# Kernel tuning notes

Hardware: AMD Instinct MI355X
Metric: run time of the kernel (lower is better)

The kernel has to match this reference:

```python
import jax, jax.numpy as jnp
import numpy as np

N = 8192      # num nodes
D = 128       # feature dim (input_dim)
E = 262144    # num edges (avg degree 32)
P = 4         # num perspectives (num_pers)
EPSILON = 0.3 # similarity threshold (args.epsilon)


def setup_inputs() -> dict:
    key = jax.random.key(0)
    k1, k2, k3, k4 = jax.random.split(key, 4)
    x = jax.random.normal(k1, (N, D), dtype=jnp.float32)
    ori_index = jax.random.randint(k2, (2, E), 0, N, dtype=jnp.int32)
    ori_weight = jax.random.uniform(k3, (E,), dtype=jnp.float32)
    w_pers = jax.random.normal(k4, (P, D), dtype=jnp.float32)  # weighted-cosine perspective weights
    return {"x": x, "ori_index": ori_index, "ori_weight": ori_weight, "w_pers": w_pers}


def reference(x, ori_index, ori_weight, w_pers):
    n = x.shape[0]
    # to_dense_adj: scatter edge weights into dense [N, N] adjacency (duplicate edges add)
    ori_g = jnp.zeros((n, n), dtype=x.dtype).at[ori_index[0], ori_index[1]].add(ori_weight)

    # GraphLearner (weighted multi-perspective cosine):
    # reweight features per perspective, L2-normalize, cosine sim, mean over perspectives
    xw = x[None, :, :] * w_pers[:, None, :]                              # [P, N, D]
    xn = xw / jnp.maximum(jnp.linalg.norm(xw, axis=-1, keepdims=True), 1e-12)
    sim = jnp.mean(jnp.einsum('pnd,pmd->pnm', xn, xn), axis=0)           # [N, N]
    # epsilon-thresholded learned graph
    sim_g = jnp.where(sim > EPSILON, sim, jnp.zeros_like(sim))

    # purified(sim, ori_g, epsilon): keep original edges where sim*ori_g > epsilon
    pur_g = jnp.where(sim * ori_g > EPSILON, ori_g, jnp.zeros_like(sim))
    new_g = pur_g + sim_g
    # dense_to_sparse has data-dependent output size; return the dense refined
    # adjacency (same information: edges = nonzero(new_g), weights = values).
    return new_g
```

## Files before the change

kernel.cpp:

```cpp
#include <hip/hip_runtime.h>
#include <hip/hip_bf16.h>
#include <stdint.h>

#define N_NODES 8192
#define DIM     128
#define KTOT    512
#define NEDGE   262144
#define EPS     0.3f
#define FIX_DELTA 0.0043f
#define FIX_CAP (1u << 19)
#define XCAP    (1u << 18)
#define LCAP    512
#define HASH_BITS 19
#define HASH_SLOTS (1u << HASH_BITS)

typedef unsigned int u32;
typedef unsigned short u16;
typedef __attribute__((ext_vector_type(8))) short short8;
typedef __attribute__((ext_vector_type(4))) float float4v;

#define OFF_YF  0u
#define OFF_YB  16777216u
#define OFF_CTR 25165824u
#define OFF_HK  25166080u
#define OFF_HV  27263232u
#define OFF_FL  29360384u
#define OFF_UL  31457536u
#define OFF_XL  32506112u
#define ZERO_VEC4 262160u

__device__ __forceinline__ u16 f2bf(float f) {
    u32 b = __builtin_bit_cast(u32, f);
    b += 0x7fffu + ((b >> 16) & 1u);
    return (u16)(b >> 16);
}

__global__ void prep_y(const float* __restrict__ x, const float* __restrict__ wp,
                       float* __restrict__ yf, u16* __restrict__ yb,
                       uint4* __restrict__ zbase) {
    if (blockIdx.x >= 2048) {
        for (u32 idx = (blockIdx.x - 2048) * 256 + threadIdx.x; idx < ZERO_VEC4;
             idx += 512 * 256)
            zbase[idx] = make_uint4(0, 0, 0, 0);
        return;
    }
    int node = blockIdx.x * 4 + (threadIdx.x >> 6);
    int lane = threadIdx.x & 63;
    float x0 = x[node * DIM + lane];
    float x1 = x[node * DIM + lane + 64];
    for (int p = 0; p < 4; ++p) {
        float v0 = x0 * wp[p * DIM + lane];
        float v1 = x1 * wp[p * DIM + lane + 64];
        float ss = v0 * v0 + v1 * v1;
        #pragma unroll
        for (int o = 1; o < 64; o <<= 1) ss += __shfl_xor(ss, o, 64);
        float scale = 0.5f / fmaxf(sqrtf(ss), 1e-12f);
        float y0 = v0 * scale, y1 = v1 * scale;
        int base = node * KTOT + p * DIM;
        yf[base + lane] = y0;       yf[base + lane + 64] = y1;
        yb[base + lane] = f2bf(y0); yb[base + lane + 64] = f2bf(y1);
    }
}

__global__ void edge_insert(const int* __restrict__ idx, const float* __restrict__ w,
                            u32* __restrict__ hkey, float* __restrict__ hval,
                            u32* __restrict__ ucnt, u32* __restrict__ ulist) {
    int e = blockIdx.x * 256 + threadIdx.x;
    u32 cell = (u32)(idx[e] * N_NODES + idx[NEDGE + e]);
    float wv = w[e];
    u32 key = cell + 1u;
    u32 h = (cell * 2654435761u) >> (32 - HASH_BITS);
    while (true) {
        u32 old = atomicCAS(&hkey[h], 0u, key);
        if (old == 0u) { ulist[atomicAdd(ucnt, 1u)] = h; atomicAdd(&hval[h], wv); break; }
        if (old == key) { atomicAdd(&hval[h], wv); break; }
        h = (h + 1u) & (HASH_SLOTS - 1u);
    }
}

#define TM  128
#define BK  64
#define TLD 132

__global__ __launch_bounds__(512)
void gemm_sim(const u16* __restrict__ yb, float* __restrict__ out,
              u32* __restrict__ fcnt, u32* __restrict__ flst) {
    int bm = blockIdx.y, bn = blockIdx.x;
    if (bm > bn) return;
    __shared__ __align__(16) char smem[64 * TLD * 4];
    u16* As = (u16*)smem;
    u16* Bs = As + TM * BK;
    float* tbuf = (float*)smem;
    __shared__ u32 s_cnt, s_base;
    __shared__ u32 s_list[LCAP];
    int tid = threadIdx.x;
    int lane = tid & 63, wid = tid >> 6;
    int wm = wid >> 1, wn = wid & 1;
    if (tid == 0) s_cnt = 0;

    float4v acc[2][4] = {};
    const u16* arow = yb + (size_t)(bm * TM) * KTOT;
    const u16* brow = yb + (size_t)(bn * TM) * KTOT;

    for (int kt = 0; kt < KTOT / BK; ++kt) {
        __syncthreads();
        #pragma unroll
        for (int q = 0; q < 2; ++q) {
            int c = q * 512 + wid * 64 + lane;
            int row = c >> 3;
            int kg = (c & 7) ^ (row & 7);
            __builtin_amdgcn_global_load_lds(
                (const __attribute__((address_space(1))) void*)(const void*)(arow + (size_t)row * KTOT + kt * BK + kg * 8),
                (__attribute__((address_space(3))) void*)(void*)(As + (q * 512 + wid * 64) * 8),
                16, 0, 0);
            __builtin_amdgcn_global_load_lds(
                (const __attribute__((address_space(1))) void*)(const void*)(brow + (size_t)row * KTOT + kt * BK + kg * 8),
                (__attribute__((address_space(3))) void*)(void*)(Bs + (q * 512 + wid * 64) * 8),
                16, 0, 0);
        }
        __syncthreads();
        #pragma unroll
        for (int kk = 0; kk < 2; ++kk) {
            short8 af[2], bfr[4];
            int kg2 = kk * 4 + (lane >> 4);
            int mrow = wm * 32 + (lane & 15);
            int ncol = wn * 64 + (lane & 15);
            #pragma unroll
            for (int i = 0; i < 2; ++i) {
                int ra = mrow + i * 16;
                af[i] = *(const short8*)&As[ra * BK + ((kg2 ^ (ra & 7)) * 8)];
            }
            #pragma unroll
            for (int j = 0; j < 4; ++j) {
                int rb = ncol + j * 16;
                bfr[j] = *(const short8*)&Bs[rb * BK + ((kg2 ^ (rb & 7)) * 8)];
            }
            #pragma unroll
            for (int i = 0; i < 2; ++i)
                #pragma unroll
                for (int j = 0; j < 4; ++j)
                    acc[i][j] = __builtin_amdgcn_mfma_f32_16x16x32_bf16(
                        af[i], bfr[j], acc[i][j], 0, 0, 0);
        }
    }

    int quad = lane >> 4, lcol = lane & 15;
    #pragma unroll
    for (int i = 0; i < 2; ++i)
        #pragma unroll
        for (int j = 0; j < 4; ++j) {
            int gr0 = bm * TM + wm * 32 + i * 16 + quad * 4;
            int gc  = bn * TM + wn * 64 + j * 16 + lcol;
            #pragma unroll
            for (int r = 0; r < 4; ++r) {
                float s = acc[i][j][r];
                __builtin_nontemporal_store(s > EPS ? s : 0.f,
                                            &out[(size_t)(gr0 + r) * N_NODES + gc]);
                if (fabsf(s - EPS) < FIX_DELTA) {
                    u32 cell = (u32)((gr0 + r) * N_NODES + gc);
                    u32 li = atomicAdd(&s_cnt, 1u);
                    if (li < LCAP) s_list[li] = cell;
                    else { u32 g = atomicAdd(fcnt, 1u); if (g < FIX_CAP) flst[g] = cell; }
                }
            }
        }

    #pragma unroll
    for (int h = 0; h < 2; ++h) {
        __syncthreads();
        if (wn == h) {
            #pragma unroll
            for (int i = 0; i < 2; ++i) {
                int Lr = wm * 32 + i * 16 + quad * 4;
                #pragma unroll
                for (int j = 0; j < 4; ++j) {
                    int Lc = j * 16 + lcol;
                    *(float4v*)&tbuf[Lc * TLD + Lr] = acc[i][j];
                }
            }
        }
        __syncthreads();
        #pragma unroll
        for (int v = 0; v < 4; ++v) {
            int chunk = v * 512 + tid;
            int row = chunk >> 5, c4 = chunk & 31;
            float4v t = *(const float4v*)&tbuf[row * TLD + c4 * 4];
            float4v o;
            #pragma unroll
            for (int r = 0; r < 4; ++r) o[r] = t[r] > EPS ? t[r] : 0.f;
            __builtin_nontemporal_store(o,
                (float4v*)&out[(size_t)(bn * TM + h * 64 + row) * N_NODES + bm * TM + c4 * 4]);
        }
    }

    __syncthreads();
    u32 cnt = s_cnt < LCAP ? s_cnt : LCAP;
    if (tid == 0) s_base = atomicAdd(fcnt, cnt);
    __syncthreads();
    for (u32 t = tid; t < cnt; t += 512) {
        u32 g = s_base + t;
        if (g < FIX_CAP) flst[g] = s_list[t];
    }
}

__device__ __forceinline__ float dot_exact(const float* __restrict__ yf,
                                           u32 i, u32 j, int tl) {
    const float4v* ri = (const float4v*)(yf + (size_t)i * KTOT);
    const float4v* rj = (const float4v*)(yf + (size_t)j * KTOT);
    float4v p = {};
    #pragma unroll
    for (int q = 0; q < 8; ++q) p += ri[q * 16 + tl] * rj[q * 16 + tl];
    float s = p.x + p.y + p.z + p.w;
    #pragma unroll
    for (int o = 8; o >= 1; o >>= 1) s += __shfl_xor(s, o, 16);
    return s;
}

__global__ void fix_and_edges(const float* __restrict__ yf,
                              const u32* __restrict__ fcnt, const u32* __restrict__ flst,
                              const u32* __restrict__ hkey, const float* __restrict__ hval,
                              const u32* __restrict__ ucnt, const u32* __restrict__ ulist,
                              float* __restrict__ out,
                              u32* __restrict__ xcnt, u32* __restrict__ xlist) {
    if (blockIdx.x < 1024) {
        u32 count = *fcnt; if (count > FIX_CAP) count = FIX_CAP;
        int team = (blockIdx.x * 256 + threadIdx.x) >> 4;
        int tl = threadIdx.x & 15;
        int nteams = 1024 * 16;
        for (u32 t = team; t < count; t += nteams) {
            u32 cell = flst[t];
            u32 i = cell >> 13, j = cell & 8191u;
            float s = dot_exact(yf, i, j, tl);
            if (tl == 0) {
                float v = s > EPS ? s : 0.f;
                out[(size_t)i * N_NODES + j] = v;
                out[(size_t)j * N_NODES + i] = v;
            }
        }
    } else {
        u32 count = *ucnt;
        for (u32 t = (blockIdx.x - 1024) * 256 + threadIdx.x; t < count; t += 512 * 256) {
            u32 h = ulist[t];
            u32 cell = hkey[h] - 1u;
            float a = hval[h];
            float sg = out[cell];
            bool hard = (a > 1.0f) ||
                        (fabsf(sg - EPS) < FIX_DELTA + 1e-6f) ||
                        (sg > 0.f && fabsf(sg * a - EPS) < FIX_DELTA * a + 1e-6f) ||
                        (sg == 0.f && a > 0.97f);
            if (hard) {
                u32 g = atomicAdd(xcnt, 1u);
                if (g < XCAP) xlist[g] = h;
            } else if (sg > 0.f) {
                out[cell] = sg + ((sg * a > EPS) ? a : 0.f);
            }
        }
    }
}

__global__ void edge_exact(const float* __restrict__ yf, const u32* __restrict__ hkey,
                           const float* __restrict__ hval, const u32* __restrict__ xcnt,
                           const u32* __restrict__ xlist, float* __restrict__ out) {
    u32 count = *xcnt; if (count > XCAP) count = XCAP;
    int team = (blockIdx.x * 256 + threadIdx.x) >> 4;
    int tl = threadIdx.x & 15;
    int nteams = gridDim.x * 16;
    for (u32 t = team; t < count; t += nteams) {
        u32 h = xlist[t];
        u32 cell = hkey[h] - 1u;
        float a = hval[h];
        u32 i = cell >> 13, j = cell & 8191u;
        float s = dot_exact(yf, i, j, tl);
        if (tl == 0) {
            float v = s > EPS ? s : 0.f;
            if (s * a > EPS) v += a;
            out[cell] = v;
        }
    }
}

extern "C" void kernel_launch(void* const* d_in, const int* in_sizes, int n_in,
                              void* d_out, int out_size, void* d_ws, size_t ws_size,
                              hipStream_t stream) {
    const float* x  = (const float*)d_in[0];
    const int*   oi = (const int*)d_in[1];
    const float* ow = (const float*)d_in[2];
    const float* wp = (const float*)d_in[3];
    float* out = (float*)d_out;
    char* ws = (char*)d_ws;
    float* yf = (float*)(ws + OFF_YF);
    u16*   yb = (u16*)(ws + OFF_YB);
    u32*   fc = (u32*)(ws + OFF_CTR);
    u32*   uc = (u32*)(ws + OFF_CTR + 4);
    u32*   xc = (u32*)(ws + OFF_CTR + 8);
    u32*   hk = (u32*)(ws + OFF_HK);
    float* hv = (float*)(ws + OFF_HV);
    u32*   fl = (u32*)(ws + OFF_FL);
    u32*   ul = (u32*)(ws + OFF_UL);
    u32*   xl = (u32*)(ws + OFF_XL);

    prep_y<<<2560, 256, 0, stream>>>(x, wp, yf, yb, (uint4*)(ws + OFF_CTR));
    edge_insert<<<NEDGE / 256, 256, 0, stream>>>(oi, ow, hk, hv, uc, ul);
    gemm_sim<<<dim3(N_NODES / TM, N_NODES / TM), 512, 0, stream>>>(yb, out, fc, fl);
    fix_and_edges<<<1536, 256, 0, stream>>>(yf, fc, fl, hk, hv, uc, ul, out, xc, xl);
    edge_exact<<<256, 256, 0, stream>>>(yf, hk, hv, xc, xl, out);
}
```

Before: 467.5 us.

## Fuse near-threshold fixups into GEMM epilogue and merge edge-exact pass

The triangular GEMM grid is remapped onto a compact 65x32 grid, so the launch no longer includes idle lower-triangle blocks. Each block now recomputes its near-threshold cells in fp32 in its own epilogue, one wave per cell, and only overflow cells go to the global list. The separate edge_exact kernel is removed: hard edge cells are collected with a wave ballot and recomputed in place. Overflow fixups skip cells that are original edges by probing the hash table. This removes one launch and the global list traffic, but adds serial fp32 dot products to the GEMM tail and tightens the sg==0 heuristic threshold, which risks correctness.

```diff
diff --git a/kernel.cpp b/kernel.cpp
--- a/kernel.cpp
+++ b/kernel.cpp
@@ -9,7 +9,6 @@
 #define EPS     0.3f
 #define FIX_DELTA 0.0043f
 #define FIX_CAP (1u << 19)
-#define XCAP    (1u << 18)
 #define LCAP    512
 #define HASH_BITS 19
 #define HASH_SLOTS (1u << HASH_BITS)
@@ -26,13 +25,33 @@
 #define OFF_HV  27263232u
 #define OFF_FL  29360384u
 #define OFF_UL  31457536u
-#define OFF_XL  32506112u
 #define ZERO_VEC4 262160u
 
 __device__ __forceinline__ u16 f2bf(float f) {
     u32 b = __builtin_bit_cast(u32, f);
     b += 0x7fffu + ((b >> 16) & 1u);
     return (u16)(b >> 16);
+}
+
+__device__ __forceinline__ float wave_dot(const float* __restrict__ yf,
+                                          u32 i, u32 j, int lane) {
+    const float4v* ri = (const float4v*)(yf + (size_t)i * KTOT);
+    const float4v* rj = (const float4v*)(yf + (size_t)j * KTOT);
+    float4v p = ri[lane] * rj[lane] + ri[64 + lane] * rj[64 + lane];
+    float s = p.x + p.y + p.z + p.w;
+    #pragma unroll
+    for (int o = 32; o >= 1; o >>= 1) s += __shfl_xor(s, o, 64);
+    return s;
+}
+
+__device__ __forceinline__ bool is_edge(const u32* __restrict__ hkey, u32 cell) {
+    u32 h = (cell * 2654435761u) >> (32 - HASH_BITS);
+    while (true) {
+        u32 k = hkey[h];
+        if (k == 0u) return false;
+        if (k == cell + 1u) return true;
+        h = (h + 1u) & (HASH_SLOTS - 1u);
+    }
 }
 
 __global__ void prep_y(const float* __restrict__ x, const float* __restrict__ wp,
@@ -83,15 +102,17 @@
 #define TLD 132
 
 __global__ __launch_bounds__(512)
-void gemm_sim(const u16* __restrict__ yb, float* __restrict__ out,
-              u32* __restrict__ fcnt, u32* __restrict__ flst) {
-    int bm = blockIdx.y, bn = blockIdx.x;
-    if (bm > bn) return;
+void gemm_sim(const u16* __restrict__ yb, const float* __restrict__ yf,
+              float* __restrict__ out, u32* __restrict__ fcnt, u32* __restrict__ flst) {
+    int r = blockIdx.y, c = blockIdx.x;
+    int bm, bn;
+    if (c < 64 - r) { bm = r;      bn = r + c; }
+    else            { bm = 63 - r; bn = bm + (c - (64 - r)); }
     __shared__ __align__(16) char smem[64 * TLD * 4];
     u16* As = (u16*)smem;
     u16* Bs = As + TM * BK;
     float* tbuf = (float*)smem;
-    __shared__ u32 s_cnt, s_base;
+    __shared__ u32 s_cnt;
     __shared__ u32 s_list[LCAP];
     int tid = threadIdx.x;
     int lane = tid & 63, wid = tid >> 6;
@@ -106,9 +127,9 @@
         __syncthreads();
         #pragma unroll
         for (int q = 0; q < 2; ++q) {
-            int c = q * 512 + wid * 64 + lane;
-            int row = c >> 3;
-            int kg = (c & 7) ^ (row & 7);
+            int cc = q * 512 + wid * 64 + lane;
+            int row = cc >> 3;
+            int kg = (cc & 7) ^ (row & 7);
             __builtin_amdgcn_global_load_lds(
                 (const __attribute__((address_space(1))) void*)(const void*)(arow + (size_t)row * KTOT + kt * BK + kg * 8),
                 (__attribute__((address_space(3))) void*)(void*)(As + (q * 512 + wid * 64) * 8),
@@ -152,12 +173,12 @@
             int gr0 = bm * TM + wm * 32 + i * 16 + quad * 4;
             int gc  = bn * TM + wn * 64 + j * 16 + lcol;
             #pragma unroll
-            for (int r = 0; r < 4; ++r) {
-                float s = acc[i][j][r];
+            for (int rr = 0; rr < 4; ++rr) {
+                float s = acc[i][j][rr];
                 __builtin_nontemporal_store(s > EPS ? s : 0.f,
-                                            &out[(size_t)(gr0 + r) * N_NODES + gc]);
+                                            &out[(size_t)(gr0 + rr) * N_NODES + gc]);
                 if (fabsf(s - EPS) < FIX_DELTA) {
-                    u32 cell = (u32)((gr0 + r) * N_NODES + gc);
+                    u32 cell = (u32)((gr0 + rr) * N_NODES + gc);
                     u32 li = atomicAdd(&s_cnt, 1u);
                     if (li < LCAP) s_list[li] = cell;
                     else { u32 g = atomicAdd(fcnt, 1u); if (g < FIX_CAP) flst[g] = cell; }
@@ -187,7 +208,7 @@
             float4v t = *(const float4v*)&tbuf[row * TLD + c4 * 4];
             float4v o;
             #pragma unroll
-            for (int r = 0; r < 4; ++r) o[r] = t[r] > EPS ? t[r] : 0.f;
+            for (int rr = 0; rr < 4; ++rr) o[rr] = t[rr] > EPS ? t[rr] : 0.f;
             __builtin_nontemporal_store(o,
                 (float4v*)&out[(size_t)(bn * TM + h * 64 + row) * N_NODES + bm * TM + c4 * 4]);
         }
@@ -195,86 +216,65 @@
 
     __syncthreads();
     u32 cnt = s_cnt < LCAP ? s_cnt : LCAP;
-    if (tid == 0) s_base = atomicAdd(fcnt, cnt);
-    __syncthreads();
-    for (u32 t = tid; t < cnt; t += 512) {
-        u32 g = s_base + t;
-        if (g < FIX_CAP) flst[g] = s_list[t];
-    }
-}
-
-__device__ __forceinline__ float dot_exact(const float* __restrict__ yf,
-                                           u32 i, u32 j, int tl) {
-    const float4v* ri = (const float4v*)(yf + (size_t)i * KTOT);
-    const float4v* rj = (const float4v*)(yf + (size_t)j * KTOT);
-    float4v p = {};
-    #pragma unroll
-    for (int q = 0; q < 8; ++q) p += ri[q * 16 + tl] * rj[q * 16 + tl];
-    float s = p.x + p.y + p.z + p.w;
-    #pragma unroll
-    for (int o = 8; o >= 1; o >>= 1) s += __shfl_xor(s, o, 16);
-    return s;
+    for (u32 t = wid; t < cnt; t += 8) {
+        u32 cell = s_list[t];
+        u32 ii = cell >> 13, jj = cell & 8191u;
+        float s = wave_dot(yf, ii, jj, lane);
+        if (lane == 0) {
+            float v = s > EPS ? s : 0.f;
+            out[(size_t)ii * N_NODES + jj] = v;
+            out[(size_t)jj * N_NODES + ii] = v;
+        }
+    }
 }
 
 __global__ void fix_and_edges(const float* __restrict__ yf,
                               const u32* __restrict__ fcnt, const u32* __restrict__ flst,
                               const u32* __restrict__ hkey, const float* __restrict__ hval,
                               const u32* __restrict__ ucnt, const u32* __restrict__ ulist,
-                              float* __restrict__ out,
-                              u32* __restrict__ xcnt, u32* __restrict__ xlist) {
+                              float* __restrict__ out) {
+    int lane = threadIdx.x & 63;
     if (blockIdx.x < 1024) {
+        u32 count = *ucnt;
+        u32 t = blockIdx.x * 256 + threadIdx.x;
+        bool valid = t < count;
+        u32 cell = 0; float a = 0.f, sg = 0.f; bool hard = false;
+        if (valid) {
+            u32 h = ulist[t];
+            cell = hkey[h] - 1u;
+            a = hval[h];
+            sg = out[cell];
+            hard = (a > 1.0f) ||
+                   (fabsf(sg - EPS) < FIX_DELTA + 1e-6f) ||
+                   (sg > 0.f && fabsf(sg * a - EPS) < FIX_DELTA * a + 1e-6f) ||
+                   (sg == 0.f && a > 0.9855f);
+            if (!hard && sg > 0.f)
+                out[cell] = sg + ((sg * a > EPS) ? a : 0.f);
+        }
+        unsigned long long m = __ballot(hard);
+        while (m) {
+            int src = __builtin_ctzll(m);
+            m &= m - 1;
+            u32 cB = __shfl(cell, src, 64);
+            float aB = __shfl(a, src, 64);
+            float s = wave_dot(yf, cB >> 13, cB & 8191u, lane);
+            if (lane == 0) {
+                float v = s > EPS ? s : 0.f;
+                if (s * aB > EPS) v += aB;
+                out[cB] = v;
+            }
+        }
+    } else {
         u32 count = *fcnt; if (count > FIX_CAP) count = FIX_CAP;
-        int team = (blockIdx.x * 256 + threadIdx.x) >> 4;
-        int tl = threadIdx.x & 15;
-        int nteams = 1024 * 16;
-        for (u32 t = team; t < count; t += nteams) {
+        u32 wv = (blockIdx.x - 1024) * 4 + (threadIdx.x >> 6);
+        for (u32 t = wv; t < count; t += 64 * 4) {
             u32 cell = flst[t];
-            u32 i = cell >> 13, j = cell & 8191u;
-            float s = dot_exact(yf, i, j, tl);
-            if (tl == 0) {
-                float v = s > EPS ? s : 0.f;
-                out[(size_t)i * N_NODES + j] = v;
-                out[(size_t)j * N_NODES + i] = v;
-            }
-        }
-    } else {
-        u32 count = *ucnt;
-        for (u32 t = (blockIdx.x - 1024) * 256 + threadIdx.x; t < count; t += 512 * 256) {
-            u32 h = ulist[t];
-            u32 cell = hkey[h] - 1u;
-            float a = hval[h];
-            float sg = out[cell];
-            bool hard = (a > 1.0f) ||
-                        (fabsf(sg - EPS) < FIX_DELTA + 1e-6f) ||
-                        (sg > 0.f && fabsf(sg * a - EPS) < FIX_DELTA * a + 1e-6f) ||
-                        (sg == 0.f && a > 0.97f);
-            if (hard) {
-                u32 g = atomicAdd(xcnt, 1u);
-                if (g < XCAP) xlist[g] = h;
-            } else if (sg > 0.f) {
-                out[cell] = sg + ((sg * a > EPS) ? a : 0.f);
-            }
-        }
-    }
-}
-
-__global__ void edge_exact(const float* __restrict__ yf, const u32* __restrict__ hkey,
-                           const float* __restrict__ hval, const u32* __restrict__ xcnt,
-                           const u32* __restrict__ xlist, float* __restrict__ out) {
-    u32 count = *xcnt; if (count > XCAP) count = XCAP;
-    int team = (blockIdx.x * 256 + threadIdx.x) >> 4;
-    int tl = threadIdx.x & 15;
-    int nteams = gridDim.x * 16;
-    for (u32 t = team; t < count; t += nteams) {
-        u32 h = xlist[t];
-        u32 cell = hkey[h] - 1u;
-        float a = hval[h];
-        u32 i = cell >> 13, j = cell & 8191u;
-        float s = dot_exact(yf, i, j, tl);
-        if (tl == 0) {
+            u32 ii = cell >> 13, jj = cell & 8191u;
+            float s = wave_dot(yf, ii, jj, lane);
             float v = s > EPS ? s : 0.f;
-            if (s * a > EPS) v += a;
-            out[cell] = v;
+            u32 mir = jj * (u32)N_NODES + ii;
+            if (lane == 0 && !is_edge(hkey, cell)) out[(size_t)ii * N_NODES + jj] = v;
+            if (lane == 1 && !is_edge(hkey, mir))  out[(size_t)jj * N_NODES + ii] = v;
         }
     }
 }
@@ -292,16 +292,13 @@
     u16*   yb = (u16*)(ws + OFF_YB);
     u32*   fc = (u32*)(ws + OFF_CTR);
     u32*   uc = (u32*)(ws + OFF_CTR + 4);
-    u32*   xc = (u32*)(ws + OFF_CTR + 8);
     u32*   hk = (u32*)(ws + OFF_HK);
     float* hv = (float*)(ws + OFF_HV);
     u32*   fl = (u32*)(ws + OFF_FL);
     u32*   ul = (u32*)(ws + OFF_UL);
-    u32*   xl = (u32*)(ws + OFF_XL);
 
     prep_y<<<2560, 256, 0, stream>>>(x, wp, yf, yb, (uint4*)(ws + OFF_CTR));
     edge_insert<<<NEDGE / 256, 256, 0, stream>>>(oi, ow, hk, hv, uc, ul);
-    gemm_sim<<<dim3(N_NODES / TM, N_NODES / TM), 512, 0, stream>>>(yb, out, fc, fl);
-    fix_and_edges<<<1536, 256, 0, stream>>>(yf, fc, fl, hk, hv, uc, ul, out, xc, xl);
-    edge_exact<<<256, 256, 0, stream>>>(yf, hk, hv, xc, xl, out);
-}
+    gemm_sim<<<dim3(65, 32), 512, 0, stream>>>(yb, yf, out, fc, fl);
+    fix_and_edges<<<1088, 256, 0, stream>>>(yf, fc, fl, hk, hv, uc, ul, out);
+}
```

Result: faster. 424.4 us (median of 2 runs) (-9.2%).
